# Kernel optimization log

Measured on AMD Instinct MI355X. Metric: run time of the kernel, lower is better.

Reference implementation:

```python
import jax, jax.numpy as jnp
import numpy as np

B, S, C = 16384, 64, 9      # batch, seq_len, input_channels (3x3 rotation, flattened)
H, BN = 128, 64             # hidden_channels, bottle_neck_channel


def setup_inputs() -> dict:
    key = jax.random.key(0)
    ks = jax.random.split(key, 12)
    t = jnp.broadcast_to(jnp.linspace(0.0, 1.0, S, dtype=jnp.float32)[None, :], (B, S))
    x = jax.random.normal(ks[0], (B, S, C), dtype=jnp.float32)
    s = lambda fi, fo: 1.0 / np.sqrt(fi)
    return {
        "t": t, "x": x,
        # CDEFunc MLP params (hidden -> bottleneck -> bottleneck -> bottleneck -> hidden*input)
        "W1": jax.random.normal(ks[1], (H, BN), jnp.float32) * s(H, BN),  "b1": jnp.zeros((BN,), jnp.float32),
        "W2": jax.random.normal(ks[2], (BN, BN), jnp.float32) * s(BN, BN), "b2": jnp.zeros((BN,), jnp.float32),
        "W3": jax.random.normal(ks[3], (BN, BN), jnp.float32) * s(BN, BN), "b3": jnp.zeros((BN,), jnp.float32),
        "W4": jax.random.normal(ks[4], (BN, H * C), jnp.float32) * s(BN, H * C), "b4": jnp.zeros((H * C,), jnp.float32),
        # initial map input -> hidden, readout hidden -> output (9D)
        "Wi": jax.random.normal(ks[5], (C, H), jnp.float32) * s(C, H), "bi": jnp.zeros((H,), jnp.float32),
        "Wo": jax.random.normal(ks[6], (H, C), jnp.float32) * s(H, C), "bo": jnp.zeros((C,), jnp.float32),
    }


def _cde_field(z, W1, b1, W2, b2, W3, b3, W4, b4):
    """f(t,z): (B,H) -> (B,H,C). 4-layer MLP, elu/elu/elu/tanh, as in CDEFunc."""
    h = jax.nn.elu(z @ W1 + b1)
    h = jax.nn.elu(h @ W2 + b2)
    h = jax.nn.elu(h @ W3 + b3)
    h = jnp.tanh(h @ W4 + b4)
    return h.reshape(z.shape[:-1] + (H, C))


def reference(t, x, W1, b1, W2, b2, W3, b3, W4, b4, Wi, bi, Wo, bo):
    # Linear interpolation of the control path X: dX/dt is constant on each knot
    # interval, matching LinearInterpolation (SO3 paths drop the time channel,
    # so the control derivative has C channels).
    t1d = t[0]                                   # (S,) shared time grid
    dt = t1d[1:] - t1d[:-1]                      # (S-1,)
    dX = (x[:, 1:] - x[:, :-1]) / dt[None, :, None]  # (B, S-1, C)

    z0 = x[:, 0] @ Wi + bi                       # initial hidden state (B, H)

    def g(z, dXk):
        # dz/dt = f(t,z) @ dX/dt  -> (B,H)
        f = _cde_field(z, W1, b1, W2, b2, W3, b3, W4, b4)
        return jnp.einsum("bhc,bc->bh", f, dXk)

    def rk4_step(z, inp):
        dXk, h = inp                             # h: interval length (scalar)
        k1 = g(z, dXk)
        k2 = g(z + 0.5 * h * k1, dXk)
        k3 = g(z + 0.5 * h * k2, dXk)
        k4 = g(z + h * k3, dXk)
        z = z + (h / 6.0) * (k1 + 2.0 * k2 + 2.0 * k3 + k4)
        return z, None

    dX_t = jnp.transpose(dX, (1, 0, 2))          # (S-1, B, C) for scan
    zT, _ = jax.lax.scan(rk4_step, z0, (dX_t, dt))
    return zT @ Wo + bo                          # (B, output_channel)
```

## Files before the change

kernel.cpp:

```cpp
#include <hip/hip_runtime.h>
#include <cstdint>
#include <cstddef>


typedef _Float16 f16;
typedef _Float16 f16x8 __attribute__((ext_vector_type(8)));
typedef float f32x4 __attribute__((ext_vector_type(4)));

#define LOG2E     1.44269504088896340736f
#define TWOLOG2E  2.88539008177792681472f

#define MFMA3(acc, ah, al, bh, bl)                                        \
  acc = __builtin_amdgcn_mfma_f32_16x16x32_f16(ah, bh, acc, 0, 0, 0);     \
  acc = __builtin_amdgcn_mfma_f32_16x16x32_f16(al, bh, acc, 0, 0, 0);     \
  acc = __builtin_amdgcn_mfma_f32_16x16x32_f16(ah, bl, acc, 0, 0, 0);

__global__ void pack_weights(const float* __restrict__ W1, const float* __restrict__ W2,
                             const float* __restrict__ W3, const float* __restrict__ W4,
                             f16* __restrict__ wp)
{
  int t = blockIdx.x * 256 + threadIdx.x;
  if (t >= 90112) return;
  float v;
  if (t < 8192) {
    int j = t & 7, lr = (t >> 3) & 63, kb = (t >> 9) & 3, nt = t >> 11;
    int k = 32*kb + 8*(lr >> 4) + j, n = 16*nt + (lr & 15);
    v = W1[k*64 + n];
  } else if (t < 12288) {
    int u = t - 8192;
    int j = u & 7, lr = (u >> 3) & 63, kb = (u >> 9) & 1, nt = u >> 10;
    int k = 32*kb + 8*(lr >> 4) + j, n = 16*nt + (lr & 15);
    v = W2[k*64 + n];
  } else if (t < 16384) {
    int u = t - 12288;
    int j = u & 7, lr = (u >> 3) & 63, kb = (u >> 9) & 1, nt = u >> 10;
    int k = 32*kb + 8*(lr >> 4) + j, n = 16*nt + (lr & 15);
    v = W3[k*64 + n];
  } else {
    int u = t - 16384;
    int j = u & 7, lr = (u >> 3) & 63, kb = (u >> 9) & 1, nt = (u >> 10) & 7, c = u >> 13;
    int k = 32*kb + 8*(lr >> 4) + j, h = 16*nt + (lr & 15);
    v = W4[k*1152 + 9*h + c];
  }
  f16 hi = (f16)v;
  wp[t] = hi;
  wp[90112 + t] = (f16)(v - (float)hi);
}

__global__ __launch_bounds__(1024, 4) void cde_main(
    const float* __restrict__ x, const f16* __restrict__ wp,
    const float* __restrict__ b1, const float* __restrict__ b2,
    const float* __restrict__ b3, const float* __restrict__ b4,
    const float* __restrict__ Wi, const float* __restrict__ bi,
    const float* __restrict__ Wo, const float* __restrict__ bo,
    float* __restrict__ out)
{
  constexpr int SH = 0, SL = 16384, HAH = 32768, HAL = 40960, HBH = 49152, HBL = 57344;
  constexpr int UT = 65536, WH = 67840, WL = 100608, B4S = 133376;
  __shared__ __attribute__((aligned(16))) char smem[137984];

  const int tid = threadIdx.x;
  const int w   = tid >> 6;
  const int l   = tid & 63;
  const int l15 = l & 15, l4 = l >> 4;
  const int mh  = w >> 2, nq = w & 3;
  const int mg  = w >> 3, cg = w & 7;
  const int b0  = blockIdx.x << 6;
  const int colG4 = (cg << 4) + l15;
  const int xorv  = (l15 & 7) << 4;

  const f16x8* wpv = reinterpret_cast<const f16x8*>(wp);
  const f16x8* wlv = wpv + 11264;

  const float b1v = b1[(nq<<4) + l15], b2v = b2[(nq<<4) + l15], b3v = b3[(nq<<4) + l15];
  const float b1x = b1v * LOG2E, b2x = b2v * LOG2E, b3x = b3v * LOG2E;

  const f32x4 zero4 = {0.f, 0.f, 0.f, 0.f};

  {
    const f32x4* wp4 = reinterpret_cast<const f32x4*>(wp);
    for (int idx = tid; idx < 2048; idx += 1024) {
      ((f32x4*)(smem + WH))[idx] = wp4[idx];
      ((f32x4*)(smem + WL))[idx] = wp4[11264 + idx];
    }
  }
  for (int idx = tid; idx < 1152; idx += 1024) {
    int h = idx / 9, c = idx - h*9;
    ((float*)(smem + B4S))[c*128 + h] = b4[idx] * TWOLOG2E;
  }
  for (int idx = tid; idx < 1152; idx += 1024) ((float*)(smem + HAH))[idx] = Wi[idx];
  if (tid < 128) ((float*)(smem + HBH))[tid] = bi[tid];
  if (tid < 576) {
    int row = tid / 9, c = tid - row*9;
    ((float*)(smem + UT))[c*64 + row] = x[(size_t)(b0 + row)*576 + c];
  }
  __syncthreads();

  f32x4 z[2], ark[2];
  {
    float wiv[9];
#pragma unroll
    for (int c = 0; c < 9; c++) wiv[c] = ((const float*)(smem + HAH))[c*128 + colG4];
    float biv = ((const float*)(smem + HBH))[colG4];
#pragma unroll
    for (int mi = 0; mi < 2; mi++) {
      f32x4 zz = {biv, biv, biv, biv};
#pragma unroll
      for (int c = 0; c < 9; c++) {
        f32x4 xv = *reinterpret_cast<const f32x4*>(smem + UT + c*256 + 128*mg + 64*mi + 16*l4);
#pragma unroll
        for (int r = 0; r < 4; r++) zz[r] = __builtin_fmaf(xv[r], wiv[c], zz[r]);
      }
      z[mi] = zz;
#pragma unroll
      for (int r = 0; r < 4; r++) {
        int row  = 32*mg + 16*mi + 4*l4 + r;
        int byte = row*256 + ((colG4*2) ^ ((row & 7) << 4));
        f16 hi = (f16)zz[r];
        *reinterpret_cast<f16*>(smem + SH + byte) = hi;
        *reinterpret_cast<f16*>(smem + SL + byte) = (f16)(zz[r] - (float)hi);
      }
    }
  }

#pragma unroll 1
  for (int k = 0; k < 63; ++k) {
    __syncthreads();
    if (tid < 576) {
      int row = tid / 9, c = tid - row*9;
      const float* p = x + (size_t)(b0 + row)*576 + (size_t)k*9 + c;
      ((float*)(smem + UT))[c*64 + row] = p[9] - p[0];
    }
#pragma unroll 1
    for (int st = 0; st < 4; ++st) {
      __syncthreads();

      {
        f32x4 acc = zero4;
#pragma unroll
        for (int kb = 0; kb < 4; kb++) {
          int wb = ((nq*4 + kb)*64 + l)*16;
          f16x8 bh = *reinterpret_cast<const f16x8*>(smem + WH + wb);
          f16x8 bl = *reinterpret_cast<const f16x8*>(smem + WL + wb);
          int row = 16*mh + l15;
          int off = row*256 + ((16*l4 + 64*kb) ^ xorv);
          f16x8 ah = *reinterpret_cast<const f16x8*>(smem + SH + off);
          f16x8 al = *reinterpret_cast<const f16x8*>(smem + SL + off);
          MFMA3(acc, ah, al, bh, bl);
        }
#pragma unroll
        for (int r = 0; r < 4; r++) {
          float pre = acc[r];
          float lin = pre + b1v;
          float e   = __builtin_amdgcn_exp2f(__builtin_fmaf(pre, LOG2E, b1x)) - 1.0f;
          float res = lin > 0.0f ? lin : e;
          int row  = 16*mh + 4*l4 + r;
          int byte = row*128 + ((((nq<<4) + l15)*2) ^ ((row & 7) << 4));
          f16 hi = (f16)res;
          *reinterpret_cast<f16*>(smem + HAH + byte) = hi;
          *reinterpret_cast<f16*>(smem + HAL + byte) = (f16)(res - (float)hi);
        }
      }
      __syncthreads();

      {
        f32x4 acc = zero4;
#pragma unroll
        for (int kb = 0; kb < 2; kb++) {
          int wb = (1024 + (nq*2 + kb)*64 + l)*16;
          f16x8 bh = *reinterpret_cast<const f16x8*>(smem + WH + wb);
          f16x8 bl = *reinterpret_cast<const f16x8*>(smem + WL + wb);
          int row = 16*mh + l15;
          int off = row*128 + ((16*l4 + 64*kb) ^ xorv);
          f16x8 ah = *reinterpret_cast<const f16x8*>(smem + HAH + off);
          f16x8 al = *reinterpret_cast<const f16x8*>(smem + HAL + off);
          MFMA3(acc, ah, al, bh, bl);
        }
#pragma unroll
        for (int r = 0; r < 4; r++) {
          float pre = acc[r];
          float lin = pre + b2v;
          float e   = __builtin_amdgcn_exp2f(__builtin_fmaf(pre, LOG2E, b2x)) - 1.0f;
          float res = lin > 0.0f ? lin : e;
          int row  = 16*mh + 4*l4 + r;
          int byte = row*128 + ((((nq<<4) + l15)*2) ^ ((row & 7) << 4));
          f16 hi = (f16)res;
          *reinterpret_cast<f16*>(smem + HBH + byte) = hi;
          *reinterpret_cast<f16*>(smem + HBL + byte) = (f16)(res - (float)hi);
        }
      }
      __syncthreads();

      {
        f32x4 acc = zero4;
#pragma unroll
        for (int kb = 0; kb < 2; kb++) {
          int wb = (1536 + (nq*2 + kb)*64 + l)*16;
          f16x8 bh = *reinterpret_cast<const f16x8*>(smem + WH + wb);
          f16x8 bl = *reinterpret_cast<const f16x8*>(smem + WL + wb);
          int row = 16*mh + l15;
          int off = row*128 + ((16*l4 + 64*kb) ^ xorv);
          f16x8 ah = *reinterpret_cast<const f16x8*>(smem + HBH + off);
          f16x8 al = *reinterpret_cast<const f16x8*>(smem + HBL + off);
          MFMA3(acc, ah, al, bh, bl);
        }
#pragma unroll
        for (int r = 0; r < 4; r++) {
          float pre = acc[r];
          float lin = pre + b3v;
          float e   = __builtin_amdgcn_exp2f(__builtin_fmaf(pre, LOG2E, b3x)) - 1.0f;
          float res = lin > 0.0f ? lin : e;
          int row  = 16*mh + 4*l4 + r;
          int byte = row*128 + ((((nq<<4) + l15)*2) ^ ((row & 7) << 4));
          f16 hi = (f16)res;
          *reinterpret_cast<f16*>(smem + HAH + byte) = hi;
          *reinterpret_cast<f16*>(smem + HAL + byte) = (f16)(res - (float)hi);
        }
      }
      __syncthreads();

      {
        f16x8 a4h[2][2], a4l[2][2];
#pragma unroll
        for (int mi = 0; mi < 2; mi++)
#pragma unroll
          for (int kb = 0; kb < 2; kb++) {
            int row = 32*mg + 16*mi + l15;
            int off = row*128 + ((16*l4 + 64*kb) ^ xorv);
            a4h[mi][kb] = *reinterpret_cast<const f16x8*>(smem + HAH + off);
            a4l[mi][kb] = *reinterpret_cast<const f16x8*>(smem + HAL + off);
          }
        f32x4 K4[2];
        K4[0] = zero4; K4[1] = zero4;

        int ib = 2048 + (cg*2)*64 + l;
        f16x8 cbh0 = wpv[ib], cbl0 = wlv[ib], cbh1 = wpv[ib + 64], cbl1 = wlv[ib + 64];
#pragma unroll 1
        for (int c = 0; c < 9; c++) {
          f16x8 bh0 = cbh0, bl0 = cbl0, bh1 = cbh1, bl1 = cbl1;
          if (c < 8) {
            int jb = 2048 + (((c + 1)*8 + cg)*2)*64 + l;
            cbh0 = wpv[jb]; cbl0 = wlv[jb]; cbh1 = wpv[jb + 64]; cbl1 = wlv[jb + 64];
          }
          f32x4 ac[2];
#pragma unroll
          for (int mi = 0; mi < 2; mi++) {
            ac[mi] = zero4;
            MFMA3(ac[mi], a4h[mi][0], a4l[mi][0], bh0, bl0);
            MFMA3(ac[mi], a4h[mi][1], a4l[mi][1], bh1, bl1);
          }
          float b4c = ((const float*)(smem + B4S))[c*128 + colG4];
#pragma unroll
          for (int mi = 0; mi < 2; mi++) {
            f32x4 uv = *reinterpret_cast<const f32x4*>(smem + UT + c*256 + 128*mg + 64*mi + 16*l4);
#pragma unroll
            for (int r = 0; r < 4; r++) {
              float tex = __builtin_amdgcn_exp2f(__builtin_fmaf(ac[mi][r], TWOLOG2E, b4c));
              float th  = __builtin_fmaf(__builtin_amdgcn_rcpf(tex + 1.0f), -2.0f, 1.0f);
              K4[mi][r] = __builtin_fmaf(th, uv[r], K4[mi][r]);
            }
          }
        }
        if (st == 0) {
#pragma unroll
          for (int mi = 0; mi < 2; mi++) ark[mi] = K4[mi];
        } else if (st == 3) {
#pragma unroll
          for (int mi = 0; mi < 2; mi++)
#pragma unroll
            for (int r = 0; r < 4; r++)
              z[mi][r] = __builtin_fmaf(ark[mi][r] + K4[mi][r], 0.166666666667f, z[mi][r]);
        } else {
#pragma unroll
          for (int mi = 0; mi < 2; mi++)
#pragma unroll
            for (int r = 0; r < 4; r++)
              ark[mi][r] = __builtin_fmaf(2.0f, K4[mi][r], ark[mi][r]);
        }
        const float alpha = (st == 2) ? 1.0f : 0.5f;
#pragma unroll
        for (int mi = 0; mi < 2; mi++)
#pragma unroll
          for (int r = 0; r < 4; r++) {
            float sv = (st == 3) ? z[mi][r] : __builtin_fmaf(alpha, K4[mi][r], z[mi][r]);
            int row  = 32*mg + 16*mi + 4*l4 + r;
            int byte = row*256 + ((colG4*2) ^ ((row & 7) << 4));
            f16 hi = (f16)sv;
            *reinterpret_cast<f16*>(smem + SH + byte) = hi;
            *reinterpret_cast<f16*>(smem + SL + byte) = (f16)(sv - (float)hi);
          }
      }
    }
  }

  __syncthreads();
#pragma unroll
  for (int mi = 0; mi < 2; mi++)
#pragma unroll
    for (int r = 0; r < 4; r++) {
      int row = 32*mg + 16*mi + 4*l4 + r;
      ((float*)smem)[row*128 + colG4] = z[mi][r];
    }
  for (int idx = tid; idx < 1152; idx += 1024) ((float*)(smem + HBH))[idx] = Wo[idx];
  __syncthreads();
  if (tid < 576) {
    int b_ = tid / 9, c = tid - b_*9;
    float acc = bo[c];
#pragma unroll 4
    for (int h = 0; h < 128; h++)
      acc = __builtin_fmaf(((const float*)smem)[b_*128 + h],
                           ((const float*)(smem + HBH))[h*9 + c], acc);
    out[(size_t)(b0 + b_)*9 + c] = acc;
  }
}

extern "C" void kernel_launch(void* const* d_in, const int* in_sizes, int n_in,
                              void* d_out, int out_size, void* d_ws, size_t ws_size,
                              hipStream_t stream)
{
  const float* x  = (const float*)d_in[1];
  const float* W1 = (const float*)d_in[2];
  const float* b1 = (const float*)d_in[3];
  const float* W2 = (const float*)d_in[4];
  const float* b2 = (const float*)d_in[5];
  const float* W3 = (const float*)d_in[6];
  const float* b3 = (const float*)d_in[7];
  const float* W4 = (const float*)d_in[8];
  const float* b4 = (const float*)d_in[9];
  const float* Wi = (const float*)d_in[10];
  const float* bi = (const float*)d_in[11];
  const float* Wo = (const float*)d_in[12];
  const float* bo = (const float*)d_in[13];
  f16* wp = (f16*)d_ws;

  pack_weights<<<352, 256, 0, stream>>>(W1, W2, W3, W4, wp);
  cde_main<<<256, 1024, 0, stream>>>(x, wp, b1, b2, b3, b4, Wi, bi, Wo, bo, (float*)d_out);
}
```

Before: 3.191 ms.

## Halve block batch tile, read layer1-3 weights from global, pipeline W4 loads

```diff
diff --git a/kernel.cpp b/kernel.cpp
--- a/kernel.cpp
+++ b/kernel.cpp
@@ -47,7 +47,35 @@
   wp[90112 + t] = (f16)(v - (float)hi);
 }
 
-__global__ __launch_bounds__(1024, 4) void cde_main(
+__device__ __forceinline__ void tanh_k4(f32x4& K, const f32x4 ac, float b4c, const f32x4 uv) {
+#pragma unroll
+  for (int r = 0; r < 4; r++) {
+    float tex = __builtin_amdgcn_exp2f(__builtin_fmaf(ac[r], TWOLOG2E, b4c));
+    float th  = __builtin_fmaf(__builtin_amdgcn_rcpf(tex + 1.0f), -2.0f, 1.0f);
+    K[r] = __builtin_fmaf(th, uv[r], K[r]);
+  }
+}
+
+#define LOADSET(P, c) do {                                                \
+    int base_ = 2048 + (((c)*8 + w)*2)*64 + l;                            \
+    P##h0 = wpv[base_];      P##l0 = wlv[base_];                          \
+    P##h1 = wpv[base_ + 64]; P##l1 = wlv[base_ + 64];                     \
+  } while (0)
+
+#define COMPUTE(P, c) do {                                                \
+    f32x4 ac0 = zero4, ac1 = zero4;                                       \
+    MFMA3(ac0, a4h[0][0], a4l[0][0], P##h0, P##l0);                       \
+    MFMA3(ac0, a4h[0][1], a4l[0][1], P##h1, P##l1);                       \
+    MFMA3(ac1, a4h[1][0], a4l[1][0], P##h0, P##l0);                       \
+    MFMA3(ac1, a4h[1][1], a4l[1][1], P##h1, P##l1);                       \
+    float b4c = ((const float*)(smem + B4S))[(c)*128 + colG4];            \
+    f32x4 uv0 = *reinterpret_cast<const f32x4*>(smem + UT + (c)*128 + 16*l4);      \
+    f32x4 uv1 = *reinterpret_cast<const f32x4*>(smem + UT + (c)*128 + 64 + 16*l4); \
+    tanh_k4(K4[0], ac0, b4c, uv0);                                        \
+    tanh_k4(K4[1], ac1, b4c, uv1);                                        \
+  } while (0)
+
+__global__ __launch_bounds__(512, 4) void cde_main(
     const float* __restrict__ x, const f16* __restrict__ wp,
     const float* __restrict__ b1, const float* __restrict__ b2,
     const float* __restrict__ b3, const float* __restrict__ b4,
@@ -55,18 +83,17 @@
     const float* __restrict__ Wo, const float* __restrict__ bo,
     float* __restrict__ out)
 {
-  constexpr int SH = 0, SL = 16384, HAH = 32768, HAL = 40960, HBH = 49152, HBL = 57344;
-  constexpr int UT = 65536, WH = 67840, WL = 100608, B4S = 133376;
-  __shared__ __attribute__((aligned(16))) char smem[137984];
+  constexpr int SH = 0, SL = 8192, HAH = 16384, HAL = 20480, HBH = 24576, HBL = 28672;
+  constexpr int UT = 32768, B4S = 33920;
+  __shared__ __attribute__((aligned(16))) char smem[38528];
 
   const int tid = threadIdx.x;
   const int w   = tid >> 6;
   const int l   = tid & 63;
   const int l15 = l & 15, l4 = l >> 4;
   const int mh  = w >> 2, nq = w & 3;
-  const int mg  = w >> 3, cg = w & 7;
-  const int b0  = blockIdx.x << 6;
-  const int colG4 = (cg << 4) + l15;
+  const int b0  = blockIdx.x << 5;
+  const int colG4 = (w << 4) + l15;
   const int xorv  = (l15 & 7) << 4;
 
   const f16x8* wpv = reinterpret_cast<const f16x8*>(wp);
@@ -77,26 +104,19 @@
 
   const f32x4 zero4 = {0.f, 0.f, 0.f, 0.f};
 
-  {
-    const f32x4* wp4 = reinterpret_cast<const f32x4*>(wp);
-    for (int idx = tid; idx < 2048; idx += 1024) {
-      ((f32x4*)(smem + WH))[idx] = wp4[idx];
-      ((f32x4*)(smem + WL))[idx] = wp4[11264 + idx];
-    }
-  }
-  for (int idx = tid; idx < 1152; idx += 1024) {
+  for (int idx = tid; idx < 1152; idx += 512) {
     int h = idx / 9, c = idx - h*9;
     ((float*)(smem + B4S))[c*128 + h] = b4[idx] * TWOLOG2E;
   }
-  for (int idx = tid; idx < 1152; idx += 1024) ((float*)(smem + HAH))[idx] = Wi[idx];
+  for (int idx = tid; idx < 1152; idx += 512) ((float*)(smem + HAH))[idx] = Wi[idx];
   if (tid < 128) ((float*)(smem + HBH))[tid] = bi[tid];
-  if (tid < 576) {
+  if (tid < 288) {
     int row = tid / 9, c = tid - row*9;
-    ((float*)(smem + UT))[c*64 + row] = x[(size_t)(b0 + row)*576 + c];
+    ((float*)(smem + UT))[c*32 + row] = x[(size_t)(b0 + row)*576 + c];
   }
   __syncthreads();
 
-  f32x4 z[2], ark[2];
+  f32x4 z[2], ark[2], K4[2];
   {
     float wiv[9];
 #pragma unroll
@@ -107,14 +127,14 @@
       f32x4 zz = {biv, biv, biv, biv};
 #pragma unroll
       for (int c = 0; c < 9; c++) {
-        f32x4 xv = *reinterpret_cast<const f32x4*>(smem + UT + c*256 + 128*mg + 64*mi + 16*l4);
+        f32x4 xv = *reinterpret_cast<const f32x4*>(smem + UT + c*128 + 64*mi + 16*l4);
 #pragma unroll
         for (int r = 0; r < 4; r++) zz[r] = __builtin_fmaf(xv[r], wiv[c], zz[r]);
       }
       z[mi] = zz;
 #pragma unroll
       for (int r = 0; r < 4; r++) {
-        int row  = 32*mg + 16*mi + 4*l4 + r;
+        int row  = 16*mi + 4*l4 + r;
         int byte = row*256 + ((colG4*2) ^ ((row & 7) << 4));
         f16 hi = (f16)zz[r];
         *reinterpret_cast<f16*>(smem + SH + byte) = hi;
@@ -125,28 +145,40 @@
 
 #pragma unroll 1
   for (int k = 0; k < 63; ++k) {
-    __syncthreads();
-    if (tid < 576) {
-      int row = tid / 9, c = tid - row*9;
-      const float* p = x + (size_t)(b0 + row)*576 + (size_t)k*9 + c;
-      ((float*)(smem + UT))[c*64 + row] = p[9] - p[0];
-    }
 #pragma unroll 1
     for (int st = 0; st < 4; ++st) {
       __syncthreads();
 
+      f16x8 w1h[4], w1l[4];
+#pragma unroll
+      for (int kb = 0; kb < 4; kb++) {
+        int i = (nq*4 + kb)*64 + l;
+        w1h[kb] = wpv[i]; w1l[kb] = wlv[i];
+      }
+
+      if (st == 0 && tid < 288) {
+        int row = tid / 9, c = tid - row*9;
+        const float* p = x + (size_t)(b0 + row)*576 + (size_t)k*9 + c;
+        ((float*)(smem + UT))[c*32 + row] = p[9] - p[0];
+      }
+
+      f16x8 w2h[2], w2l[2], w3h[2], w3l[2];
+      f16x8 Ah0, Al0, Ah1, Al1, Bh0, Bl0, Bh1, Bl1;
+
       {
         f32x4 acc = zero4;
 #pragma unroll
         for (int kb = 0; kb < 4; kb++) {
-          int wb = ((nq*4 + kb)*64 + l)*16;
-          f16x8 bh = *reinterpret_cast<const f16x8*>(smem + WH + wb);
-          f16x8 bl = *reinterpret_cast<const f16x8*>(smem + WL + wb);
           int row = 16*mh + l15;
           int off = row*256 + ((16*l4 + 64*kb) ^ xorv);
           f16x8 ah = *reinterpret_cast<const f16x8*>(smem + SH + off);
           f16x8 al = *reinterpret_cast<const f16x8*>(smem + SL + off);
-          MFMA3(acc, ah, al, bh, bl);
+          MFMA3(acc, ah, al, w1h[kb], w1l[kb]);
+        }
+#pragma unroll
+        for (int kb = 0; kb < 2; kb++) {
+          int i = 1024 + (nq*2 + kb)*64 + l;
+          w2h[kb] = wpv[i]; w2l[kb] = wlv[i];
         }
 #pragma unroll
         for (int r = 0; r < 4; r++) {
@@ -167,14 +199,16 @@
         f32x4 acc = zero4;
 #pragma unroll
         for (int kb = 0; kb < 2; kb++) {
-          int wb = (1024 + (nq*2 + kb)*64 + l)*16;
-          f16x8 bh = *reinterpret_cast<const f16x8*>(smem + WH + wb);
-          f16x8 bl = *reinterpret_cast<const f16x8*>(smem + WL + wb);
           int row = 16*mh + l15;
           int off = row*128 + ((16*l4 + 64*kb) ^ xorv);
           f16x8 ah = *reinterpret_cast<const f16x8*>(smem + HAH + off);
           f16x8 al = *reinterpret_cast<const f16x8*>(smem + HAL + off);
-          MFMA3(acc, ah, al, bh, bl);
+          MFMA3(acc, ah, al, w2h[kb], w2l[kb]);
+        }
+#pragma unroll
+        for (int kb = 0; kb < 2; kb++) {
+          int i = 1536 + (nq*2 + kb)*64 + l;
+          w3h[kb] = wpv[i]; w3l[kb] = wlv[i];
         }
 #pragma unroll
         for (int r = 0; r < 4; r++) {
@@ -195,15 +229,13 @@
         f32x4 acc = zero4;
 #pragma unroll
         for (int kb = 0; kb < 2; kb++) {
-          int wb = (1536 + (nq*2 + kb)*64 + l)*16;
-          f16x8 bh = *reinterpret_cast<const f16x8*>(smem + WH + wb);
-          f16x8 bl = *reinterpret_cast<const f16x8*>(smem + WL + wb);
           int row = 16*mh + l15;
           int off = row*128 + ((16*l4 + 64*kb) ^ xorv);
           f16x8 ah = *reinterpret_cast<const f16x8*>(smem + HBH + off);
           f16x8 al = *reinterpret_cast<const f16x8*>(smem + HBL + off);
-          MFMA3(acc, ah, al, bh, bl);
-        }
+          MFMA3(acc, ah, al, w3h[kb], w3l[kb]);
+        }
+        LOADSET(A, 0);
 #pragma unroll
         for (int r = 0; r < 4; r++) {
           float pre = acc[r];
@@ -225,42 +257,23 @@
         for (int mi = 0; mi < 2; mi++)
 #pragma unroll
           for (int kb = 0; kb < 2; kb++) {
-            int row = 32*mg + 16*mi + l15;
+            int row = 16*mi + l15;
             int off = row*128 + ((16*l4 + 64*kb) ^ xorv);
             a4h[mi][kb] = *reinterpret_cast<const f16x8*>(smem + HAH + off);
             a4l[mi][kb] = *reinterpret_cast<const f16x8*>(smem + HAL + off);
           }
-        f32x4 K4[2];
         K4[0] = zero4; K4[1] = zero4;
 
-        int ib = 2048 + (cg*2)*64 + l;
-        f16x8 cbh0 = wpv[ib], cbl0 = wlv[ib], cbh1 = wpv[ib + 64], cbl1 = wlv[ib + 64];
+        LOADSET(B, 1);
 #pragma unroll 1
-        for (int c = 0; c < 9; c++) {
-          f16x8 bh0 = cbh0, bl0 = cbl0, bh1 = cbh1, bl1 = cbl1;
-          if (c < 8) {
-            int jb = 2048 + (((c + 1)*8 + cg)*2)*64 + l;
-            cbh0 = wpv[jb]; cbl0 = wlv[jb]; cbh1 = wpv[jb + 64]; cbl1 = wlv[jb + 64];
-          }
-          f32x4 ac[2];
-#pragma unroll
-          for (int mi = 0; mi < 2; mi++) {
-            ac[mi] = zero4;
-            MFMA3(ac[mi], a4h[mi][0], a4l[mi][0], bh0, bl0);
-            MFMA3(ac[mi], a4h[mi][1], a4l[mi][1], bh1, bl1);
-          }
-          float b4c = ((const float*)(smem + B4S))[c*128 + colG4];
-#pragma unroll
-          for (int mi = 0; mi < 2; mi++) {
-            f32x4 uv = *reinterpret_cast<const f32x4*>(smem + UT + c*256 + 128*mg + 64*mi + 16*l4);
-#pragma unroll
-            for (int r = 0; r < 4; r++) {
-              float tex = __builtin_amdgcn_exp2f(__builtin_fmaf(ac[mi][r], TWOLOG2E, b4c));
-              float th  = __builtin_fmaf(__builtin_amdgcn_rcpf(tex + 1.0f), -2.0f, 1.0f);
-              K4[mi][r] = __builtin_fmaf(th, uv[r], K4[mi][r]);
-            }
-          }
-        }
+        for (int cc = 0; cc < 4; ++cc) {
+          COMPUTE(A, 2*cc);
+          LOADSET(A, 2*cc + 2);
+          COMPUTE(B, 2*cc + 1);
+          if (cc < 3) LOADSET(B, 2*cc + 3);
+        }
+        COMPUTE(A, 8);
+
         if (st == 0) {
 #pragma unroll
           for (int mi = 0; mi < 2; mi++) ark[mi] = K4[mi];
@@ -283,7 +296,7 @@
 #pragma unroll
           for (int r = 0; r < 4; r++) {
             float sv = (st == 3) ? z[mi][r] : __builtin_fmaf(alpha, K4[mi][r], z[mi][r]);
-            int row  = 32*mg + 16*mi + 4*l4 + r;
+            int row  = 16*mi + 4*l4 + r;
             int byte = row*256 + ((colG4*2) ^ ((row & 7) << 4));
             f16 hi = (f16)sv;
             *reinterpret_cast<f16*>(smem + SH + byte) = hi;
@@ -298,18 +311,18 @@
   for (int mi = 0; mi < 2; mi++)
 #pragma unroll
     for (int r = 0; r < 4; r++) {
-      int row = 32*mg + 16*mi + 4*l4 + r;
+      int row = 16*mi + 4*l4 + r;
       ((float*)smem)[row*128 + colG4] = z[mi][r];
     }
-  for (int idx = tid; idx < 1152; idx += 1024) ((float*)(smem + HBH))[idx] = Wo[idx];
+  for (int idx = tid; idx < 1152; idx += 512) ((float*)(smem + HAH))[idx] = Wo[idx];
   __syncthreads();
-  if (tid < 576) {
+  if (tid < 288) {
     int b_ = tid / 9, c = tid - b_*9;
     float acc = bo[c];
 #pragma unroll 4
     for (int h = 0; h < 128; h++)
       acc = __builtin_fmaf(((const float*)smem)[b_*128 + h],
-                           ((const float*)(smem + HBH))[h*9 + c], acc);
+                           ((const float*)(smem + HAH))[h*9 + c], acc);
     out[(size_t)(b0 + b_)*9 + c] = acc;
   }
 }
@@ -334,5 +347,5 @@
   f16* wp = (f16*)d_ws;
 
   pack_weights<<<352, 256, 0, stream>>>(W1, W2, W3, W4, wp);
-  cde_main<<<256, 1024, 0, stream>>>(x, wp, b1, b2, b3, b4, Wi, bi, Wo, bo, (float*)d_out);
+  cde_main<<<512, 512, 0, stream>>>(x, wp, b1, b2, b3, b4, Wi, bi, Wo, bo, (float*)d_out);
 }
```

New measurement: 5.825 ms. +82.6%, slower.
